# Kernel tuning notes

Hardware: AMD Instinct MI355X
Metric: run time of the kernel (lower is better)

## Reference

```python
import jax, jax.numpy as jnp
import numpy as np

N = 100_000   # nodes
E = 1_000_000 # edges
F = 128       # nfeat
H = 2         # heads
C = 64        # nhid (per-head out channels)
NEG_SLOPE = 0.2
BN_EPS = 1e-5


def setup_inputs() -> dict:
    key = jax.random.key(0)
    ks = jax.random.split(key, 6)
    x = jax.random.normal(ks[0], (N, F), dtype=jnp.float32)
    edge_index = jax.random.randint(ks[1], (2, E), 0, N, dtype=jnp.int32)
    # GATConv params (xavier-ish scale)
    W = jax.random.normal(ks[2], (F, H * C), dtype=jnp.float32) * np.float32(1.0 / np.sqrt(F))
    att_src = jax.random.normal(ks[3], (H, C), dtype=jnp.float32) * np.float32(0.1)
    att_dst = jax.random.normal(ks[4], (H, C), dtype=jnp.float32) * np.float32(0.1)
    bias = jnp.zeros((H * C,), dtype=jnp.float32)
    # BatchNorm1d affine params
    gamma = jnp.ones((H * C,), dtype=jnp.float32)
    beta = jnp.zeros((H * C,), dtype=jnp.float32)
    return {"x": x, "edge_index": edge_index, "W": W, "att_src": att_src,
            "att_dst": att_dst, "bias": bias, "gamma": gamma, "beta": beta}


def reference(x, edge_index, W, att_src, att_dst, bias, gamma, beta):
    n = x.shape[0]
    # --- GATConv (PyG semantics): add self-loops, per-head linear, edge attention ---
    loop = jnp.arange(n, dtype=edge_index.dtype)
    src = jnp.concatenate([edge_index[0], loop])  # message sources (j)
    dst = jnp.concatenate([edge_index[1], loop])  # aggregation targets (i)

    h = (x @ W).reshape(n, H, C)                      # [N,H,C]
    a_src = jnp.einsum('nhc,hc->nh', h, att_src)      # [N,H]
    a_dst = jnp.einsum('nhc,hc->nh', h, att_dst)      # [N,H]

    e = jax.nn.leaky_relu(a_src[src] + a_dst[dst], NEG_SLOPE)  # [Et,H]
    # segment softmax over incoming edges of each dst node
    m = jax.lax.stop_gradient(jax.ops.segment_max(e, dst, num_segments=n))
    e = jnp.exp(e - m[dst])
    s = jax.ops.segment_sum(e, dst, num_segments=n)
    alpha = e / s[dst]                                 # [Et,H]

    out = jax.ops.segment_sum(alpha[:, :, None] * h[src], dst, num_segments=n)  # [N,H,C]
    out = out.reshape(n, H * C) + bias                 # concat heads + bias

    # --- transition: ReLU -> BatchNorm1d (training-mode batch stats) -> Dropout(eval=identity) ---
    out = jax.nn.relu(out)
    mean = out.mean(axis=0)
    var = out.var(axis=0)  # biased, as BN uses for normalization
    out = gamma * (out - mean) * jax.lax.rsqrt(var + BN_EPS) + beta
    return out
```

## Files before the change

### kernel.cpp

```cpp
#include <hip/hip_runtime.h>

#define NN 100000
#define EE 1000000
#define ET (EE + NN)
#define HC 128
#define NB 391
#define AGG_BLOCKS 2048
#define NGRP (NN / 4)
#define NTILE 6250
#define GEMM_BLKS 768

typedef __attribute__((ext_vector_type(8))) short short8;
typedef __attribute__((ext_vector_type(4))) float f32x4;

__device__ __forceinline__ unsigned bfpack(float a, float b) {
    unsigned ua = __float_as_uint(a), ub = __float_as_uint(b);
    ua += 0x7fff + ((ua >> 16) & 1);
    ub += 0x7fff + ((ub >> 16) & 1);
    return (ua >> 16) | (ub & 0xffff0000u);
}

__global__ __launch_bounds__(64) void k_wprep(const float* __restrict__ W,
                                              uint4* __restrict__ wf)
{
    const int bid = blockIdx.x;
    const int ks = bid >> 3, nt = bid & 7;
    const int l = threadIdx.x;
    const int n = nt * 16 + (l & 15);
    const int k0 = ks * 32 + (l >> 4) * 8;
    unsigned u[4];
    #pragma unroll
    for (int r = 0; r < 4; ++r)
        u[r] = bfpack(W[(k0 + 2*r) * HC + n], W[(k0 + 2*r + 1) * HC + n]);
    wf[bid * 64 + l] = make_uint4(u[0], u[1], u[2], u[3]);
}

__global__ __launch_bounds__(256) void k_gemmhist(
    const float* __restrict__ x, const uint4* __restrict__ wf,
    const float* __restrict__ atts, const float* __restrict__ attd,
    unsigned* __restrict__ hB, float2* __restrict__ asrc2, float2* __restrict__ adst2,
    const int* __restrict__ ei, int* __restrict__ hist)
{
    __shared__ uint4 wl[2048];

    if (blockIdx.x >= GEMM_BLKS) {
        const int t0 = (blockIdx.x - GEMM_BLKS) * 256 + threadIdx.x;
        for (int t = t0; t < ET; t += 256 * 256) {
            int d = (t < EE) ? ei[EE + t] : (t - EE);
            atomicAdd(&hist[d], 1);
        }
        return;
    }

    for (int i = threadIdx.x; i < 2048; i += 256) wl[i] = wf[i];
    __syncthreads();

    const int wv = threadIdx.x >> 6, lane = threadIdx.x & 63;
    const int g = lane >> 4, c15 = lane & 15;

    float As[8], Ad[8];
    #pragma unroll
    for (int nt = 0; nt < 8; ++nt) {
        As[nt] = atts[nt * 16 + c15];
        Ad[nt] = attd[nt * 16 + c15];
    }

    for (int t = blockIdx.x * 4 + wv; t < NTILE; t += GEMM_BLKS * 4) {
        const int row0 = t * 16;
        union { unsigned u[4]; short8 v; } af[4];
        const float* xr = x + (size_t)(row0 + c15) * HC + g * 8;
        #pragma unroll
        for (int ks = 0; ks < 4; ++ks) {
            float4 lo = *(const float4*)(xr + ks * 32);
            float4 hi = *(const float4*)(xr + ks * 32 + 4);
            af[ks].u[0] = bfpack(lo.x, lo.y);
            af[ks].u[1] = bfpack(lo.z, lo.w);
            af[ks].u[2] = bfpack(hi.x, hi.y);
            af[ks].u[3] = bfpack(hi.z, hi.w);
        }
        f32x4 acc[8];
        #pragma unroll
        for (int nt = 0; nt < 8; ++nt) acc[nt] = (f32x4)(0.f);
        #pragma unroll
        for (int nt = 0; nt < 8; ++nt) {
            #pragma unroll
            for (int ks = 0; ks < 4; ++ks) {
                short8 bfr = *(const short8*)&wl[(ks * 8 + nt) * 64 + lane];
                acc[nt] = __builtin_amdgcn_mfma_f32_16x16x32_bf16(
                    af[ks].v, bfr, acc[nt], 0, 0, 0);
            }
        }
        #pragma unroll
        for (int r = 0; r < 4; ++r) {
            const int row = row0 + g * 4 + r;
            float ps = 0.f, pd = 0.f, qs = 0.f, qd = 0.f;
            #pragma unroll
            for (int nt = 0; nt < 4; ++nt) {
                float a = acc[nt][r], b = acc[nt + 4][r];
                hB[(size_t)row * 64 + nt * 16 + c15] = bfpack(a, b);
                ps += a * As[nt];     qs += a * Ad[nt];
                pd += b * As[nt + 4]; qd += b * Ad[nt + 4];
            }
            for (int off = 8; off; off >>= 1) {
                ps += __shfl_xor(ps, off); pd += __shfl_xor(pd, off);
                qs += __shfl_xor(qs, off); qd += __shfl_xor(qd, off);
            }
            if (c15 == 0) {
                asrc2[row] = make_float2(ps, pd);
                adst2[row] = make_float2(qs, qd);
            }
        }
    }
}

__device__ __forceinline__ void edge_sd(const int* __restrict__ ei, int t, int& s, int& d) {
    if (t < EE) { s = ei[t]; d = ei[EE + t]; }
    else        { s = t - EE; d = t - EE; }
}

__global__ __launch_bounds__(256) void k_scan1(const int* __restrict__ hist,
                                               int* __restrict__ part)
{
    __shared__ int ls[256];
    int i = blockIdx.x * 256 + threadIdx.x;
    ls[threadIdx.x] = (i < NN) ? hist[i] : 0;
    __syncthreads();
    for (int off = 128; off; off >>= 1) {
        if (threadIdx.x < off) ls[threadIdx.x] += ls[threadIdx.x + off];
        __syncthreads();
    }
    if (!threadIdx.x) part[blockIdx.x] = ls[0];
}

__global__ __launch_bounds__(512) void k_scan2(int* __restrict__ part)
{
    __shared__ int ls[512];
    int tid = threadIdx.x;
    int v = (tid < NB) ? part[tid] : 0;
    ls[tid] = v;
    __syncthreads();
    for (int off = 1; off < 512; off <<= 1) {
        int t = (tid >= off) ? ls[tid - off] : 0;
        __syncthreads();
        ls[tid] += t;
        __syncthreads();
    }
    if (tid < NB) part[tid] = ls[tid] - v;
}

__global__ __launch_bounds__(256) void k_scan3(const int* __restrict__ hist,
                                               const int* __restrict__ part,
                                               int* __restrict__ row_ptr)
{
    __shared__ int ls[256];
    int i = blockIdx.x * 256 + threadIdx.x;
    int v = (i < NN) ? hist[i] : 0;
    ls[threadIdx.x] = v;
    __syncthreads();
    for (int off = 1; off < 256; off <<= 1) {
        int t = (threadIdx.x >= off) ? ls[threadIdx.x - off] : 0;
        __syncthreads();
        ls[threadIdx.x] += t;
        __syncthreads();
    }
    if (i < NN) row_ptr[i] = part[blockIdx.x] + ls[threadIdx.x] - v;
    if (i == 0) row_ptr[NN] = ET;
}

__global__ __launch_bounds__(256) void k_bucket(
    const int* __restrict__ ei, const float* __restrict__ asrc,
    const float* __restrict__ adst, const int* __restrict__ row_ptr,
    int* __restrict__ cursor, uint2* __restrict__ csr8)
{
    int t = blockIdx.x * 256 + threadIdx.x;
    if (t >= ET) return;
    int s, d; edge_sd(ei, t, s, d);
    float2 av = *(const float2*)&asrc[s * 2];
    float2 dv = *(const float2*)&adst[d * 2];
    float e0 = av.x + dv.x; e0 = e0 > 0.f ? e0 : 0.2f * e0;
    float e1 = av.y + dv.y; e1 = e1 > 0.f ? e1 : 0.2f * e1;
    int pos = row_ptr[d] + atomicAdd(&cursor[d], 1);
    csr8[pos] = make_uint2((unsigned)s, bfpack(__expf(e0), __expf(e1)));
}

__device__ __forceinline__ void gather8x2(const unsigned* base, const unsigned* off,
                                          unsigned long long* w) {
    asm volatile(
        "global_load_dwordx2 %0, %8,  %16\n\t"
        "global_load_dwordx2 %1, %9,  %16\n\t"
        "global_load_dwordx2 %2, %10, %16\n\t"
        "global_load_dwordx2 %3, %11, %16\n\t"
        "global_load_dwordx2 %4, %12, %16\n\t"
        "global_load_dwordx2 %5, %13, %16\n\t"
        "global_load_dwordx2 %6, %14, %16\n\t"
        "global_load_dwordx2 %7, %15, %16\n\t"
        "s_waitcnt vmcnt(0)"
        : "=&v"(w[0]), "=&v"(w[1]), "=&v"(w[2]), "=&v"(w[3]),
          "=&v"(w[4]), "=&v"(w[5]), "=&v"(w[6]), "=&v"(w[7])
        : "v"(off[0]), "v"(off[1]), "v"(off[2]), "v"(off[3]),
          "v"(off[4]), "v"(off[5]), "v"(off[6]), "v"(off[7]),
          "s"(base)
        : "memory");
}

__global__ __launch_bounds__(256) void k_agg(
    const int* __restrict__ row_ptr, const uint2* __restrict__ csr8,
    const unsigned* __restrict__ hB, const float* __restrict__ bias,
    float* __restrict__ out, float* __restrict__ bpart)
{
    __shared__ float lsum[HC], lsq[HC];
    __shared__ int    lidx[4][64];
    __shared__ float2 lp[4][64];
    const int tid = threadIdx.x;
    if (tid < HC) { lsum[tid] = 0.f; lsq[tid] = 0.f; }
    __syncthreads();

    const int wv = tid >> 6, lane = tid & 63;
    const int half = lane >> 5, m = lane & 31;
    const float bA0 = bias[2*m],      bB0 = bias[2*m + 1];
    const float bA1 = bias[2*m + 64], bB1 = bias[2*m + 65];

    for (int g = blockIdx.x; g < NGRP; g += AGG_BLOCKS) {
        const int node = g * 4 + wv;
        const int beg = row_ptr[node], end = row_ptr[node + 1];

        float s0 = 0.f, s1 = 0.f;
        float a0 = 0.f, a1 = 0.f, b0 = 0.f, b1 = 0.f;

        for (int base = beg; base < end; base += 64) {
            const int cnt = min(64, end - base);
            if (lane < cnt) {
                uint2 e = csr8[base + lane];
                float2 pv = make_float2(__uint_as_float(e.y << 16),
                                        __uint_as_float(e.y & 0xffff0000u));
                lidx[wv][lane] = (int)e.x;
                lp[wv][lane] = pv;
                s0 += pv.x; s1 += pv.y;
            }
            for (int j0 = 0; j0 < cnt; j0 += 16) {
                unsigned off[8]; unsigned long long w[8];
                float px[8], py[8];
                #pragma unroll
                for (int u = 0; u < 8; ++u) {
                    int j  = j0 + 2 * u + half;
                    int jc = j < cnt ? j : cnt - 1;
                    int s  = lidx[wv][jc];
                    float2 pv = lp[wv][jc];
                    px[u] = j < cnt ? pv.x : 0.f;
                    py[u] = j < cnt ? pv.y : 0.f;
                    off[u] = ((unsigned)s * 64u + (unsigned)m * 2u) * 4u;
                }
                gather8x2(hB, off, w);
                #pragma unroll
                for (int u = 0; u < 8; ++u) {
                    unsigned wlo = (unsigned)w[u];
                    unsigned whi = (unsigned)(w[u] >> 32);
                    a0 = fmaf(px[u], __uint_as_float(wlo << 16),          a0);
                    a1 = fmaf(py[u], __uint_as_float(wlo & 0xffff0000u),  a1);
                    b0 = fmaf(px[u], __uint_as_float(whi << 16),          b0);
                    b1 = fmaf(py[u], __uint_as_float(whi & 0xffff0000u),  b1);
                }
            }
        }

        a0 += __shfl_xor(a0, 32); a1 += __shfl_xor(a1, 32);
        b0 += __shfl_xor(b0, 32); b1 += __shfl_xor(b1, 32);
        for (int o = 32; o; o >>= 1) {
            s0 += __shfl_xor(s0, o);
            s1 += __shfl_xor(s1, o);
        }
        const float i0 = 1.f / s0, i1 = 1.f / s1;

        if (half == 0) {
            float vA0 = a0 * i0 + bA0; vA0 = vA0 > 0.f ? vA0 : 0.f;
            float vB0 = b0 * i0 + bB0; vB0 = vB0 > 0.f ? vB0 : 0.f;
            float vA1 = a1 * i1 + bA1; vA1 = vA1 > 0.f ? vA1 : 0.f;
            float vB1 = b1 * i1 + bB1; vB1 = vB1 > 0.f ? vB1 : 0.f;
            *(float2*)&out[(size_t)node * HC + 2*m]      = make_float2(vA0, vB0);
            *(float2*)&out[(size_t)node * HC + 64 + 2*m] = make_float2(vA1, vB1);
            atomicAdd(&lsum[2*m],      vA0); atomicAdd(&lsq[2*m],      vA0 * vA0);
            atomicAdd(&lsum[2*m + 1],  vB0); atomicAdd(&lsq[2*m + 1],  vB0 * vB0);
            atomicAdd(&lsum[2*m + 64], vA1); atomicAdd(&lsq[2*m + 64], vA1 * vA1);
            atomicAdd(&lsum[2*m + 65], vB1); atomicAdd(&lsq[2*m + 65], vB1 * vB1);
        }
    }

    __syncthreads();
    bpart[(size_t)blockIdx.x * 256 + tid] = tid < HC ? lsum[tid] : lsq[tid - HC];
}

__global__ __launch_bounds__(256) void k_red(const float* __restrict__ bpart,
                                             float* __restrict__ p2)
{
    const int tid = threadIdx.x;
    float acc = 0.f;
    const int r0 = blockIdx.x * (AGG_BLOCKS / 16);
    #pragma unroll 4
    for (int r = 0; r < AGG_BLOCKS / 16; ++r)
        acc += bpart[(size_t)(r0 + r) * 256 + tid];
    p2[blockIdx.x * 256 + tid] = acc;
}

__global__ void k_bnparam(const float* __restrict__ p2,
                          const float* __restrict__ gamma, const float* __restrict__ beta,
                          float* __restrict__ scsh)
{
    int c = threadIdx.x;
    float sum = 0.f, sq = 0.f;
    #pragma unroll
    for (int i = 0; i < 16; ++i) {
        sum += p2[i * 256 + c];
        sq  += p2[i * 256 + c + 128];
    }
    float mean = sum * (1.f / NN);
    float var  = sq * (1.f / NN) - mean * mean;
    float sc   = gamma[c] * rsqrtf(var + 1e-5f);
    scsh[c]       = sc;
    scsh[128 + c] = beta[c] - mean * sc;
}

__global__ __launch_bounds__(256) void k_apply(float* __restrict__ out,
                                               const float* __restrict__ scsh)
{
    size_t i = (size_t)blockIdx.x * 256 + threadIdx.x;
    if (i * 4 >= (size_t)NN * HC) return;
    float4 v = ((float4*)out)[i];
    int c = (int)((i * 4) & (HC - 1));
    v.x = v.x * scsh[c]     + scsh[128 + c];
    v.y = v.y * scsh[c + 1] + scsh[128 + c + 1];
    v.z = v.z * scsh[c + 2] + scsh[128 + c + 2];
    v.w = v.w * scsh[c + 3] + scsh[128 + c + 3];
    ((float4*)out)[i] = v;
}

extern "C" void kernel_launch(void* const* d_in, const int* in_sizes, int n_in,
                              void* d_out, int out_size, void* d_ws, size_t ws_size,
                              hipStream_t stream) {
    const float* x     = (const float*)d_in[0];
    const int*   ei    = (const int*)  d_in[1];
    const float* W     = (const float*)d_in[2];
    const float* atts  = (const float*)d_in[3];
    const float* attd  = (const float*)d_in[4];
    const float* bias  = (const float*)d_in[5];
    const float* gamma = (const float*)d_in[6];
    const float* beta  = (const float*)d_in[7];
    float* out = (float*)d_out;
    float* ws  = (float*)d_ws;

    unsigned* hB     = (unsigned*)ws;
    float*    asrc   = ws + 6400000;
    float*    adst   = ws + 6600000;
    int*      hist   = (int*)(ws + 6800000);
    int*      cursor = (int*)(ws + 6900000);
    float*    scsh   = ws + 7000256;
    int*      row_ptr= (int*)(ws + 7000512);
    int*      part   = (int*)(ws + 7100513);
    uint2*    csr8   = (uint2*)(ws + 7101026);
    float*    bpart  = ws + 9301026;
    float*    p2     = ws + 9825314;
    uint4*    wf     = (uint4*)(ws + 9829412);

    hipMemsetAsync(hist, 0, (size_t)200000 * sizeof(int), stream);

    k_wprep   <<<32, 64, 0, stream>>>(W, wf);
    k_gemmhist<<<1024, 256, 0, stream>>>(x, wf, atts, attd, hB,
                                         (float2*)asrc, (float2*)adst, ei, hist);
    k_scan1   <<<NB, 256, 0, stream>>>(hist, part);
    k_scan2   <<<1, 512, 0, stream>>>(part);
    k_scan3   <<<NB, 256, 0, stream>>>(hist, part, row_ptr);
    k_bucket  <<<(ET + 255) / 256, 256, 0, stream>>>(ei, asrc, adst, row_ptr,
                                                     cursor, csr8);
    k_agg     <<<AGG_BLOCKS, 256, 0, stream>>>(row_ptr, csr8, hB, bias,
                                               out, bpart);
    k_red     <<<16, 256, 0, stream>>>(bpart, p2);
    k_bnparam <<<1, 128, 0, stream>>>(p2, gamma, beta, scsh);
    k_apply   <<<(NN * HC / 4 + 255) / 256, 256, 0, stream>>>(out, scsh);
}
```

Measured before the change: 311.3 us.

## Fold small kernels into neighbors and use hardware bf16 pack instruction

Removes three tiny launches: the weight-prep kernel moves into the GEMM block prologue, the single-block scan of partials is recomputed redundantly per block inside scan3, and the BN-parameter kernel merges into the apply kernel, which now uses a 2048-block grid-stride loop. The software round-to-nearest bf16 packing is swapped for the v_cvt_pk_bf16_f32 instruction. The aim is to cut launch and serialization gaps between dependent small kernels. The cost is redundant work: each GEMM block reconverts W from global memory, and every scan3 and apply block repeats the small scans and reductions.

Measured after the change: 299.5 us (median of 2 runs). -3.8%, faster.

```diff
diff --git a/kernel.cpp b/kernel.cpp
--- a/kernel.cpp
+++ b/kernel.cpp
@@ -13,30 +13,14 @@
 typedef __attribute__((ext_vector_type(8))) short short8;
 typedef __attribute__((ext_vector_type(4))) float f32x4;
 
-__device__ __forceinline__ unsigned bfpack(float a, float b) {
-    unsigned ua = __float_as_uint(a), ub = __float_as_uint(b);
-    ua += 0x7fff + ((ua >> 16) & 1);
-    ub += 0x7fff + ((ub >> 16) & 1);
-    return (ua >> 16) | (ub & 0xffff0000u);
-}
-
-__global__ __launch_bounds__(64) void k_wprep(const float* __restrict__ W,
-                                              uint4* __restrict__ wf)
-{
-    const int bid = blockIdx.x;
-    const int ks = bid >> 3, nt = bid & 7;
-    const int l = threadIdx.x;
-    const int n = nt * 16 + (l & 15);
-    const int k0 = ks * 32 + (l >> 4) * 8;
-    unsigned u[4];
-    #pragma unroll
-    for (int r = 0; r < 4; ++r)
-        u[r] = bfpack(W[(k0 + 2*r) * HC + n], W[(k0 + 2*r + 1) * HC + n]);
-    wf[bid * 64 + l] = make_uint4(u[0], u[1], u[2], u[3]);
+__device__ __forceinline__ unsigned cvtpk(float a, float b) {
+    unsigned r;
+    asm("v_cvt_pk_bf16_f32 %0, %1, %2" : "=v"(r) : "v"(a), "v"(b));
+    return r;
 }
 
 __global__ __launch_bounds__(256) void k_gemmhist(
-    const float* __restrict__ x, const uint4* __restrict__ wf,
+    const float* __restrict__ x, const float* __restrict__ W,
     const float* __restrict__ atts, const float* __restrict__ attd,
     unsigned* __restrict__ hB, float2* __restrict__ asrc2, float2* __restrict__ adst2,
     const int* __restrict__ ei, int* __restrict__ hist)
@@ -52,7 +36,16 @@
         return;
     }
 
-    for (int i = threadIdx.x; i < 2048; i += 256) wl[i] = wf[i];
+    for (int i = threadIdx.x; i < 2048; i += 256) {
+        const int bid = i >> 6, l = i & 63;
+        const int ks = bid >> 3, nt = bid & 7;
+        const int n = nt * 16 + (l & 15);
+        const int k0 = ks * 32 + (l >> 4) * 8;
+        wl[i] = make_uint4(cvtpk(W[(k0 + 0) * HC + n], W[(k0 + 1) * HC + n]),
+                           cvtpk(W[(k0 + 2) * HC + n], W[(k0 + 3) * HC + n]),
+                           cvtpk(W[(k0 + 4) * HC + n], W[(k0 + 5) * HC + n]),
+                           cvtpk(W[(k0 + 6) * HC + n], W[(k0 + 7) * HC + n]));
+    }
     __syncthreads();
 
     const int wv = threadIdx.x >> 6, lane = threadIdx.x & 63;
@@ -73,10 +66,10 @@
         for (int ks = 0; ks < 4; ++ks) {
             float4 lo = *(const float4*)(xr + ks * 32);
             float4 hi = *(const float4*)(xr + ks * 32 + 4);
-            af[ks].u[0] = bfpack(lo.x, lo.y);
-            af[ks].u[1] = bfpack(lo.z, lo.w);
-            af[ks].u[2] = bfpack(hi.x, hi.y);
-            af[ks].u[3] = bfpack(hi.z, hi.w);
+            af[ks].u[0] = cvtpk(lo.x, lo.y);
+            af[ks].u[1] = cvtpk(lo.z, lo.w);
+            af[ks].u[2] = cvtpk(hi.x, hi.y);
+            af[ks].u[3] = cvtpk(hi.z, hi.w);
         }
         f32x4 acc[8];
         #pragma unroll
@@ -97,7 +90,7 @@
             #pragma unroll
             for (int nt = 0; nt < 4; ++nt) {
                 float a = acc[nt][r], b = acc[nt + 4][r];
-                hB[(size_t)row * 64 + nt * 16 + c15] = bfpack(a, b);
+                hB[(size_t)row * 64 + nt * 16 + c15] = cvtpk(a, b);
                 ps += a * As[nt];     qs += a * Ad[nt];
                 pd += b * As[nt + 4]; qd += b * Ad[nt + 4];
             }
@@ -132,38 +125,38 @@
     if (!threadIdx.x) part[blockIdx.x] = ls[0];
 }
 
-__global__ __launch_bounds__(512) void k_scan2(int* __restrict__ part)
-{
-    __shared__ int ls[512];
-    int tid = threadIdx.x;
-    int v = (tid < NB) ? part[tid] : 0;
+__global__ __launch_bounds__(256) void k_scan3(const int* __restrict__ hist,
+                                               const int* __restrict__ part,
+                                               int* __restrict__ row_ptr)
+{
+    __shared__ int ls[256];
+    __shared__ int bofs[NB];
+    const int tid = threadIdx.x;
+    if (tid < 64) {
+        int carry = 0;
+        for (int c = 0; c < NB; c += 64) {
+            const int idx = c + tid;
+            int v = (idx < NB) ? part[idx] : 0;
+            const int orig = v;
+            for (int o = 1; o < 64; o <<= 1) {
+                int u = __shfl_up(v, o);
+                if (tid >= o) v += u;
+            }
+            if (idx < NB) bofs[idx] = carry + v - orig;
+            carry += __shfl(v, 63);
+        }
+    }
+    int i = blockIdx.x * 256 + tid;
+    int v = (i < NN) ? hist[i] : 0;
     ls[tid] = v;
     __syncthreads();
-    for (int off = 1; off < 512; off <<= 1) {
+    for (int off = 1; off < 256; off <<= 1) {
         int t = (tid >= off) ? ls[tid - off] : 0;
         __syncthreads();
         ls[tid] += t;
         __syncthreads();
     }
-    if (tid < NB) part[tid] = ls[tid] - v;
-}
-
-__global__ __launch_bounds__(256) void k_scan3(const int* __restrict__ hist,
-                                               const int* __restrict__ part,
-                                               int* __restrict__ row_ptr)
-{
-    __shared__ int ls[256];
-    int i = blockIdx.x * 256 + threadIdx.x;
-    int v = (i < NN) ? hist[i] : 0;
-    ls[threadIdx.x] = v;
-    __syncthreads();
-    for (int off = 1; off < 256; off <<= 1) {
-        int t = (threadIdx.x >= off) ? ls[threadIdx.x - off] : 0;
-        __syncthreads();
-        ls[threadIdx.x] += t;
-        __syncthreads();
-    }
-    if (i < NN) row_ptr[i] = part[blockIdx.x] + ls[threadIdx.x] - v;
+    if (i < NN) row_ptr[i] = bofs[blockIdx.x] + ls[tid] - v;
     if (i == 0) row_ptr[NN] = ET;
 }
 
@@ -180,7 +173,7 @@
     float e0 = av.x + dv.x; e0 = e0 > 0.f ? e0 : 0.2f * e0;
     float e1 = av.y + dv.y; e1 = e1 > 0.f ? e1 : 0.2f * e1;
     int pos = row_ptr[d] + atomicAdd(&cursor[d], 1);
-    csr8[pos] = make_uint2((unsigned)s, bfpack(__expf(e0), __expf(e1)));
+    csr8[pos] = make_uint2((unsigned)s, cvtpk(__expf(e0), __expf(e1)));
 }
 
 __device__ __forceinline__ void gather8x2(const unsigned* base, const unsigned* off,
@@ -301,36 +294,36 @@
     p2[blockIdx.x * 256 + tid] = acc;
 }
 
-__global__ void k_bnparam(const float* __restrict__ p2,
-                          const float* __restrict__ gamma, const float* __restrict__ beta,
-                          float* __restrict__ scsh)
-{
-    int c = threadIdx.x;
-    float sum = 0.f, sq = 0.f;
-    #pragma unroll
-    for (int i = 0; i < 16; ++i) {
-        sum += p2[i * 256 + c];
-        sq  += p2[i * 256 + c + 128];
-    }
-    float mean = sum * (1.f / NN);
-    float var  = sq * (1.f / NN) - mean * mean;
-    float sc   = gamma[c] * rsqrtf(var + 1e-5f);
-    scsh[c]       = sc;
-    scsh[128 + c] = beta[c] - mean * sc;
-}
-
-__global__ __launch_bounds__(256) void k_apply(float* __restrict__ out,
-                                               const float* __restrict__ scsh)
-{
-    size_t i = (size_t)blockIdx.x * 256 + threadIdx.x;
-    if (i * 4 >= (size_t)NN * HC) return;
-    float4 v = ((float4*)out)[i];
-    int c = (int)((i * 4) & (HC - 1));
-    v.x = v.x * scsh[c]     + scsh[128 + c];
-    v.y = v.y * scsh[c + 1] + scsh[128 + c + 1];
-    v.z = v.z * scsh[c + 2] + scsh[128 + c + 2];
-    v.w = v.w * scsh[c + 3] + scsh[128 + c + 3];
-    ((float4*)out)[i] = v;
+__global__ __launch_bounds__(256) void k_apply(
+    const float* __restrict__ p2, const float* __restrict__ gamma,
+    const float* __restrict__ beta, float* __restrict__ out)
+{
+    __shared__ float scsh[256];
+    const int tid = threadIdx.x;
+    if (tid < HC) {
+        float sum = 0.f, sq = 0.f;
+        #pragma unroll
+        for (int i = 0; i < 16; ++i) {
+            sum += p2[i * 256 + tid];
+            sq  += p2[i * 256 + tid + 128];
+        }
+        float mean = sum * (1.f / NN);
+        float var  = sq * (1.f / NN) - mean * mean;
+        float sc   = gamma[tid] * rsqrtf(var + 1e-5f);
+        scsh[tid]       = sc;
+        scsh[128 + tid] = beta[tid] - mean * sc;
+    }
+    __syncthreads();
+    for (size_t i = (size_t)blockIdx.x * 256 + tid; i < (size_t)NN * HC / 4;
+         i += (size_t)gridDim.x * 256) {
+        float4 v = ((float4*)out)[i];
+        int c = (int)((i * 4) & (HC - 1));
+        v.x = v.x * scsh[c]     + scsh[128 + c];
+        v.y = v.y * scsh[c + 1] + scsh[128 + c + 1];
+        v.z = v.z * scsh[c + 2] + scsh[128 + c + 2];
+        v.w = v.w * scsh[c + 3] + scsh[128 + c + 3];
+        ((float4*)out)[i] = v;
+    }
 }
 
 extern "C" void kernel_launch(void* const* d_in, const int* in_sizes, int n_in,
@@ -352,27 +345,22 @@
     float*    adst   = ws + 6600000;
     int*      hist   = (int*)(ws + 6800000);
     int*      cursor = (int*)(ws + 6900000);
-    float*    scsh   = ws + 7000256;
     int*      row_ptr= (int*)(ws + 7000512);
     int*      part   = (int*)(ws + 7100513);
     uint2*    csr8   = (uint2*)(ws + 7101026);
     float*    bpart  = ws + 9301026;
     float*    p2     = ws + 9825314;
-    uint4*    wf     = (uint4*)(ws + 9829412);
 
     hipMemsetAsync(hist, 0, (size_t)200000 * sizeof(int), stream);
 
-    k_wprep   <<<32, 64, 0, stream>>>(W, wf);
-    k_gemmhist<<<1024, 256, 0, stream>>>(x, wf, atts, attd, hB,
+    k_gemmhist<<<1024, 256, 0, stream>>>(x, W, atts, attd, hB,
                                          (float2*)asrc, (float2*)adst, ei, hist);
     k_scan1   <<<NB, 256, 0, stream>>>(hist, part);
-    k_scan2   <<<1, 512, 0, stream>>>(part);
     k_scan3   <<<NB, 256, 0, stream>>>(hist, part, row_ptr);
     k_bucket  <<<(ET + 255) / 256, 256, 0, stream>>>(ei, asrc, adst, row_ptr,
                                                      cursor, csr8);
     k_agg     <<<AGG_BLOCKS, 256, 0, stream>>>(row_ptr, csr8, hB, bias,
                                                out, bpart);
     k_red     <<<16, 256, 0, stream>>>(bpart, p2);
-    k_bnparam <<<1, 128, 0, stream>>>(p2, gamma, beta, scsh);
-    k_apply   <<<(NN * HC / 4 + 255) / 256, 256, 0, stream>>>(out, scsh);
-}
+    k_apply   <<<2048, 256, 0, stream>>>(p2, gamma, beta, out);
+}
```
